# Performance work log

Hardware: AMD Instinct MI355X
Metric: run time of the kernel (lower is better)

## Reference

```python
import jax, jax.numpy as jnp
import numpy as np

NUM_EMBEDDINGS = 8192
EMBEDDING_DIM = 256
BETA = 0.25


def setup_inputs() -> dict:
    key = jax.random.key(0)
    k1, k2 = jax.random.split(key)
    z = jax.random.normal(k1, (16, 256, 32, 32), dtype=jnp.float32)
    # torch init: uniform(-1/K, 1/K)
    emb_w = jax.random.uniform(k2, (NUM_EMBEDDINGS, EMBEDDING_DIM),
                               dtype=jnp.float32,
                               minval=-1.0 / NUM_EMBEDDINGS,
                               maxval=1.0 / NUM_EMBEDDINGS)
    return {"z": z, "emb_w": emb_w}


def reference(z, emb_w):
    B, C, H, W = z.shape
    z_bhwc = jnp.transpose(z, (0, 2, 3, 1))          # [B,H,W,C]
    flat = z_bhwc.reshape(-1, C)                      # [N,C]
    d = (jnp.sum(flat * flat, axis=1, keepdims=True)
         + jnp.sum(emb_w * emb_w, axis=1)
         - 2.0 * flat @ emb_w.T)                      # [N,K]
    idx = jnp.argmin(d, axis=1)                       # [N]
    # direct gather (mathematically identical to one-hot @ emb_w)
    quantized = emb_w[idx].reshape(z_bhwc.shape)      # [B,H,W,C]
    q_latent_loss = jnp.mean((jax.lax.stop_gradient(quantized) - z_bhwc) ** 2)
    e_latent_loss = jnp.mean((quantized - jax.lax.stop_gradient(z_bhwc)) ** 2)
    loss = q_latent_loss + BETA * e_latent_loss
    # straight-through estimator
    quantized_st = z_bhwc + jax.lax.stop_gradient(quantized - z_bhwc)
    out = jnp.transpose(quantized_st, (0, 3, 1, 2))   # [B,C,H,W]
    return out, loss, idx.reshape(B, -1)
```

## Files before the change

### kernel.cpp

```cpp
#include <hip/hip_runtime.h>
#include <cstdint>
#include <cstddef>

#define N_PIX   16384
#define K_EMB   8192
#define DDIM    256

#define WS_A8       0
#define WS_E8       4194304
#define WS_KEYS     6291456
#define WS_ZSQ      23068672
#define WS_ESQ      23134208
#define WS_LOSS     23166976
#define WS_CNT      23166984

typedef float f32x4 __attribute__((ext_vector_type(4)));

__device__ __forceinline__ unsigned int f32_sortable(float f) {
    unsigned int u = __float_as_uint(f);
    return (u & 0x80000000u) ? ~u : (u | 0x80000000u);
}

__device__ __forceinline__ unsigned char f2fp8(float x) {
    unsigned ub = __float_as_uint(x);
    unsigned sgn = (ub >> 24) & 0x80u;
    unsigned b = ub & 0x7FFFFFFFu;
    unsigned out;
    if (__uint_as_float(b) < 0.015625f) {
        out = (unsigned)(int)rintf(__uint_as_float(b) * 512.0f);
    } else {
        unsigned r = b + 0x7FFFFu + ((b >> 20) & 1u);
        int er = (int)(r >> 23) - 127;
        out = (unsigned)(((er + 7) << 3) | ((r >> 20) & 7u));
    }
    return (unsigned char)(out | sgn);
}

#if defined(__has_builtin)
#if __has_builtin(__builtin_amdgcn_cvt_pk_fp8_f32)
#define HAVE_CVT_FP8 1
#endif
#endif

__device__ __forceinline__ unsigned pack4_fp8(float a, float b, float c, float d) {
#ifdef HAVE_CVT_FP8
    int pk = 0;
    pk = __builtin_amdgcn_cvt_pk_fp8_f32(a, b, pk, false);
    pk = __builtin_amdgcn_cvt_pk_fp8_f32(c, d, pk, true);
    return (unsigned)pk;
#else
    return (unsigned)f2fp8(a) | ((unsigned)f2fp8(b) << 8)
         | ((unsigned)f2fp8(c) << 16) | ((unsigned)f2fp8(d) << 24);
#endif
}

__device__ __forceinline__ void async16(const unsigned char* g, unsigned char* l) {
    __builtin_amdgcn_global_load_lds(
        (const __attribute__((address_space(1))) void*)g,
        (__attribute__((address_space(3))) void*)l, 16, 0, 0);
}

__device__ __forceinline__ float np_pairwise_sq256(const float* row) {
    float r[16];
#pragma unroll
    for (int j = 0; j < 16; ++j) r[j] = 0.f;
#pragma unroll
    for (int c = 0; c < 256; ++c) {
        float x  = row[c];
        float sq = __fmul_rn(x, x);
        int slot = ((c >> 7) << 3) | (c & 7);
        r[slot] = __fadd_rn(r[slot], sq);
    }
    float h0 = __fadd_rn(
        __fadd_rn(__fadd_rn(r[0], r[1]), __fadd_rn(r[2], r[3])),
        __fadd_rn(__fadd_rn(r[4], r[5]), __fadd_rn(r[6], r[7])));
    float h1 = __fadd_rn(
        __fadd_rn(__fadd_rn(r[8], r[9]), __fadd_rn(r[10], r[11])),
        __fadd_rn(__fadd_rn(r[12], r[13]), __fadd_rn(r[14], r[15])));
    return __fadd_rn(h0, h1);
}

__device__ __forceinline__ size_t cm_addr(int r, int c) {
    int ks = c >> 5;
    int h  = (c >> 4) & 1;
    int s  = h ^ ((r >> 2) & 1);
    return (size_t)ks * 4096 + (size_t)r * 32 + s * 16 + (c & 15);
}

__global__ __launch_bounds__(256) void prep_kernel(
        const float* __restrict__ z, const float* __restrict__ emb,
        unsigned char* __restrict__ Af8, unsigned char* __restrict__ Ef8,
        float* __restrict__ zsq, float* __restrict__ esq,
        double* __restrict__ lossAcc, unsigned* __restrict__ doneCnt) {
    __shared__ float tile[32][257];
    int blk = blockIdx.x;
    int t   = threadIdx.x;
    if (blk < 512) {
        int b   = blk >> 5;
        int hw0 = (blk & 31) * 32;
        const float* zb = z + (size_t)b * 262144 + hw0;
        int c0  = t >> 3;
        int px4 = t & 7;
#pragma unroll
        for (int cc = 0; cc < 8; ++cc) {
            int c = cc * 32 + c0;
            float4 v = *(const float4*)&zb[(size_t)c * 1024 + px4 * 4];
            tile[px4 * 4 + 0][c] = v.x;
            tile[px4 * 4 + 1][c] = v.y;
            tile[px4 * 4 + 2][c] = v.z;
            tile[px4 * 4 + 3][c] = v.w;
        }
        __syncthreads();
        int p0 = b * 1024 + hw0;
        int wv = t >> 6, lane = t & 63;
#pragma unroll
        for (int iter = 0; iter < 8; ++iter) {
            int pl = iter * 4 + wv;
            unsigned pk = pack4_fp8(tile[pl][lane * 4 + 0], tile[pl][lane * 4 + 1],
                                    tile[pl][lane * 4 + 2], tile[pl][lane * 4 + 3]);
            int p  = p0 + pl;
            int mb = p >> 7, r = p & 127;
            *(unsigned*)(Af8 + (size_t)mb * 32768 + cm_addr(r, lane * 4)) = pk;
        }
        if (t < 32) zsq[p0 + t] = np_pairwise_sq256(tile[t]);
        if (blk == 0 && t == 0) { *lossAcc = 0.0; *doneCnt = 0u; }
    } else {
        int k0 = (blk - 512) * 32;
        const float4* eg = (const float4*)(emb + (size_t)k0 * DDIM);
#pragma unroll
        for (int i = 0; i < 8; ++i) {
            int idx = i * 256 + t;
            int row = idx >> 6, c4 = idx & 63;
            float4 v = eg[idx];
            *(float4*)&tile[row][c4 * 4] = v;
        }
        __syncthreads();
#pragma unroll
        for (int i = 0; i < 8; ++i) {
            int idx = i * 256 + t;
            int row = idx >> 6, c4 = idx & 63;
            const float* rp = &tile[row][c4 * 4];
            int kg = k0 + row;
            int nb = kg >> 7, rr = kg & 127;
            *(unsigned*)(Ef8 + (size_t)nb * 32768 + cm_addr(rr, c4 * 4)) =
                pack4_fp8(rp[0] * 8192.0f, rp[1] * 8192.0f,
                          rp[2] * 8192.0f, rp[3] * 8192.0f);
        }
        if (t < 32) esq[k0 + t] = np_pairwise_sq256(tile[t]);
    }
}

__device__ __forceinline__ unsigned pack_key(float w) {
    float uf = __builtin_fmaf(w, -512.0f, 262144.0f);
    uf = fminf(uf, 524287.0f);
    unsigned u = (unsigned)uf;
    return (u << 13) | (__float_as_uint(w) & 0x1FFFu);
}

__global__ __launch_bounds__(256) void mfma_score_kernel(
        const unsigned char* __restrict__ Af8,
        const unsigned char* __restrict__ Ef8,
        unsigned int* __restrict__ keys) {
    union SM {
        struct { unsigned char As[8][4096]; unsigned char Bs[8][4096]; } k;
        struct { uint2 ep[128][33]; } e;
    };
    __shared__ SM sm;

    const int g  = blockIdx.x;
    const int mb = blockIdx.y;
    const int t = threadIdx.x;
    const int w = t >> 6, lane = t & 63;
    const int wm = w >> 1, wn = w & 1;
    const int quad = lane >> 4, l16 = lane & 15;

    const unsigned char* Ag = Af8 + (size_t)mb * 32768 + t * 16;
#pragma unroll
    for (int ks = 0; ks < 8; ++ks)
        async16(Ag + ks * 4096, &sm.k.As[ks][t * 16]);
    {
        const unsigned char* Eg = Ef8 + (size_t)(g * 4) * 32768 + t * 16;
#pragma unroll
        for (int ks = 0; ks < 8; ++ks)
            async16(Eg + ks * 4096, &sm.k.Bs[ks][t * 16]);
    }

    int aaddr[4], baddr[4];
#pragma unroll
    for (int fi = 0; fi < 4; ++fi) {
        int row = wm * 64 + fi * 16 + l16;
        int gg  = (quad >> 1) ^ ((row >> 2) & 1);
        aaddr[fi] = row * 32 + gg * 16 + (quad & 1) * 8;
    }
#pragma unroll
    for (int fj = 0; fj < 4; ++fj) {
        int row = wn * 64 + fj * 16 + l16;
        int gg  = (quad >> 1) ^ ((row >> 2) & 1);
        baddr[fj] = row * 32 + gg * 16 + (quad & 1) * 8;
    }

    __syncthreads();

    long long afr[4][8];
#pragma unroll
    for (int fi = 0; fi < 4; ++fi)
#pragma unroll
        for (int ks = 0; ks < 8; ++ks)
            afr[fi][ks] = *(const long long*)&sm.k.As[ks][aaddr[fi]];

    const float NEGINF = __int_as_float(0xFF800000);
    float t2a[16], t2b[16];
#pragma unroll
    for (int i = 0; i < 16; ++i) { t2a[i] = NEGINF; t2b[i] = NEGINF; }

#pragma unroll 1
    for (int j = 0; j < 4; ++j) {
        f32x4 acc[4][4];
#pragma unroll
        for (int i = 0; i < 4; ++i)
#pragma unroll
            for (int jj = 0; jj < 4; ++jj)
#pragma unroll
                for (int r = 0; r < 4; ++r) acc[i][jj][r] = 0.f;

#pragma unroll
        for (int ks = 0; ks < 8; ++ks) {
            long long bfr[4];
#pragma unroll
            for (int fj = 0; fj < 4; ++fj)
                bfr[fj] = *(const long long*)&sm.k.Bs[ks][baddr[fj]];
            __builtin_amdgcn_s_setprio(1);
#pragma unroll
            for (int fi = 0; fi < 4; ++fi)
#pragma unroll
                for (int fj = 0; fj < 4; ++fj)
                    acc[fi][fj] = __builtin_amdgcn_mfma_f32_16x16x32_fp8_fp8(
                        afr[fi][ks], bfr[fj], acc[fi][fj], 0, 0, 0);
            __builtin_amdgcn_s_setprio(0);
        }
        __syncthreads();

        if (j < 3) {
            const unsigned char* Eg =
                Ef8 + (size_t)(g * 4 + j + 1) * 32768 + t * 16;
#pragma unroll
            for (int ks = 0; ks < 8; ++ks)
                async16(Eg + ks * 4096, &sm.k.Bs[ks][t * 16]);
        }

        const int nb = g * 4 + j;
        const unsigned idx0 = (unsigned)(nb * 128 + wn * 64 + l16);
#pragma unroll
        for (int fi = 0; fi < 4; ++fi) {
#pragma unroll
            for (int r = 0; r < 4; ++r) {
                const int ai = fi * 4 + r;
                float a0 = t2a[ai], b0 = t2b[ai];
#pragma unroll
                for (int fj = 0; fj < 4; ++fj) {
                    float v = acc[fi][fj][r];
                    float wv = __uint_as_float(
                        (__float_as_uint(v) & 0xFFFFE000u) | (idx0 + fj * 16));
                    float mn = fminf(a0, wv);
                    a0 = fmaxf(a0, wv);
                    b0 = fmaxf(b0, mn);
                }
                t2a[ai] = a0; t2b[ai] = b0;
            }
        }
        __syncthreads();
    }

#pragma unroll
    for (int fi = 0; fi < 4; ++fi) {
#pragma unroll
        for (int r = 0; r < 4; ++r) {
            const int ai = fi * 4 + r;
            int row = wm * 64 + fi * 16 + quad * 4 + r;
            sm.e.ep[row][wn * 16 + l16] =
                make_uint2(pack_key(t2a[ai]), pack_key(t2b[ai]));
        }
    }
    __syncthreads();

    {
        int row = t >> 1, half = t & 1, h0 = half * 16;
        uint2 mv = sm.e.ep[row][h0];
#pragma unroll
        for (int i = 1; i < 16; ++i) {
            uint2 av = sm.e.ep[row][h0 + i];
            unsigned n0 = min(mv.x, av.x);
            unsigned n1 = min(max(mv.x, av.x), min(mv.y, av.y));
            mv.x = n0; mv.y = n1;
        }
        ((uint2*)keys)[(size_t)(g * 2 + half) * N_PIX + (mb * 128 + row)] = mv;
    }
}

__global__ __launch_bounds__(256) void final_kernel(
        const unsigned int* __restrict__ keys,
        const float* __restrict__ z, const float* __restrict__ emb,
        const float* __restrict__ zsq, const float* __restrict__ esq,
        float* __restrict__ out, float* __restrict__ idx_out,
        float* __restrict__ loss_out,
        double* __restrict__ lossAcc, unsigned* __restrict__ doneCnt) {
    __shared__ float ztile[16][260];
    __shared__ uint2 kt[16][33];
    __shared__ int   scand[16][64];
    __shared__ unsigned long long ckey[1024];
    __shared__ int   soff[17];
    __shared__ int   scnt[16];
    __shared__ int   pxmap[1024];
    __shared__ float szs[16];
    __shared__ int   sidx[16];

    int blk = blockIdx.x;
    int b = blk >> 6, hh = blk & 63;
    int t = threadIdx.x;
    int p0 = b * 1024 + hh * 16;
    const float* zb = z + (size_t)b * 262144 + hh * 16;
    {
        int px = t & 15, cb = t >> 4;
#pragma unroll
        for (int cc = 0; cc < 16; ++cc) {
            int c = cc * 16 + cb;
            ztile[px][c] = zb[(size_t)c * 1024 + px];
        }
    }
    {
        const uint2* kg = (const uint2*)keys;
#pragma unroll
        for (int itr = 0; itr < 2; ++itr) {
            int idx = itr * 256 + t;
            int px = idx & 15, hf = idx >> 4;
            kt[px][hf] = kg[(size_t)hf * N_PIX + p0 + px];
        }
    }
    if (t < 16) szs[t] = zsq[p0 + t];
    __syncthreads();

    {
        int wq = t >> 6, lane = t & 63;
#pragma unroll 1
        for (int i = 0; i < 4; ++i) {
            int px = wq * 4 + i;
            uint2 ka = (lane < 32) ? kt[px][lane] : make_uint2(~0u, ~0u);
            unsigned m = min(ka.x, ka.y);
#pragma unroll
            for (int off = 32; off >= 1; off >>= 1)
                m = min(m, (unsigned)__shfl_xor((int)m, off, 64));
            unsigned thr = (m >> 13) + 1600;

            bool h0 = (lane < 32) && ((ka.x >> 13) <= thr);
            bool h1 = (lane < 32) && ((ka.y >> 13) <= thr);
            unsigned long long m0 = __ballot(h0);
            unsigned long long m1 = __ballot(h1);
            int c0 = __popcll(m0);
            unsigned long long below = (lane == 63) ? ~0ull >> 1
                                     : ((1ull << lane) - 1);
            if (h0) scand[px][__popcll(m0 & below)] = (int)(ka.x & 0x1FFFu);
            if (h1) scand[px][c0 + __popcll(m1 & below)] = (int)(ka.y & 0x1FFFu);
            if (lane == 0) scnt[px] = c0 + __popcll(m1);
        }
    }
    __syncthreads();

    if (t < 64) {
        int v = (t < 16) ? scnt[t] : 0;
#pragma unroll
        for (int o = 1; o < 16; o <<= 1) {
            int u = __shfl_up(v, o, 64);
            if (t >= o) v += u;
        }
        if (t < 16) soff[t + 1] = v;
        if (t == 0) soff[0] = 0;
    }
    __syncthreads();
    int total = soff[16];
    for (int f = t; f < total; f += 256) {
        int lo = 0, hi = 15;
        while (lo < hi) {
            int mid = (lo + hi + 1) >> 1;
            if (soff[mid] <= f) lo = mid; else hi = mid - 1;
        }
        pxmap[f] = lo;
    }
    __syncthreads();

    {
        int gid = t >> 4, l16 = t & 15;
        const float4* emb4 = (const float4*)emb;
#pragma unroll 1
        for (int f = gid; f < total; f += 16) {
            int px = pxmap[f];
            int k  = scand[px][f - soff[px]];
            double d = 0.0;
#pragma unroll
            for (int q = 0; q < 4; ++q) {
                float4 ev = emb4[(size_t)k * 64 + q * 16 + l16];
                const float* zp = &ztile[px][(q * 16 + l16) * 4];
                d += (double)zp[0] * ev.x + (double)zp[1] * ev.y
                   + (double)zp[2] * ev.z + (double)zp[3] * ev.w;
            }
#pragma unroll
            for (int o = 1; o < 16; o <<= 1) d += __shfl_xor(d, o, 64);
            if (l16 == 0) {
                float df = (float)d;
                float s  = __fsub_rn(__fadd_rn(szs[px], esq[k]),
                                     __fmul_rn(2.0f, df));
                ckey[f] = ((unsigned long long)f32_sortable(s) << 32)
                        | (unsigned)k;
            }
        }
    }
    __syncthreads();

    {
        int cpx = t >> 4, ci = t & 15;
        unsigned long long best = ~0ull;
        for (int f = soff[cpx] + ci; f < soff[cpx + 1]; f += 16) {
            unsigned long long v = ckey[f];
            best = v < best ? v : best;
        }
#pragma unroll
        for (int o = 1; o < 16; o <<= 1) {
            unsigned long long ov =
                (unsigned long long)__shfl_xor((long long)best, o, 64);
            best = ov < best ? ov : best;
        }
        if (ci == 0) {
            int k = (int)(unsigned)(best & 0xffffffffu);
            sidx[cpx] = k;
            idx_out[p0 + cpx] = (float)k;
        }
    }
    __syncthreads();

    int px2 = t & 15, cy = t >> 4;
    int kk = sidx[px2];
    const float* er = emb + (size_t)kk * DDIM;
    float* ob = out + (size_t)b * 262144 + hh * 16;
    float local = 0.f;
#pragma unroll 4
    for (int it = 0; it < 16; ++it) {
        int c = it * 16 + cy;
        float q = er[c];
        float d = q - ztile[px2][c];
        ob[(size_t)c * 1024 + px2] = q;
        local += d * d;
    }
#pragma unroll
    for (int off = 32; off >= 1; off >>= 1) local += __shfl_down(local, off, 64);
    __shared__ float wsum[4];
    if ((t & 63) == 0) wsum[t >> 6] = local;
    __syncthreads();
    if (t == 0) {
        double s = (double)wsum[0] + (double)wsum[1]
                 + (double)wsum[2] + (double)wsum[3];
        atomicAdd(lossAcc, s);
        __threadfence();
        unsigned old = atomicAdd(doneCnt, 1u);
        if (old == 1023u) {
            double tot = atomicAdd(lossAcc, 0.0);
            *loss_out = (float)(tot * (1.25 / 4194304.0));
        }
    }
}

extern "C" void kernel_launch(void* const* d_in, const int* in_sizes, int n_in,
                              void* d_out, int out_size, void* d_ws, size_t ws_size,
                              hipStream_t stream) {
    const float* z   = (const float*)d_in[0];
    const float* emb = (const float*)d_in[1];
    float* out = (float*)d_out;
    char* ws = (char*)d_ws;

    unsigned char* Af8 = (unsigned char*)(ws + WS_A8);
    unsigned char* Ef8 = (unsigned char*)(ws + WS_E8);
    unsigned int* keys = (unsigned int*)(ws + WS_KEYS);
    float* zsq      = (float*)(ws + WS_ZSQ);
    float* esq      = (float*)(ws + WS_ESQ);
    double* lossAcc = (double*)(ws + WS_LOSS);
    unsigned* doneCnt = (unsigned*)(ws + WS_CNT);

    prep_kernel<<<768, 256, 0, stream>>>(z, emb, Af8, Ef8, zsq, esq,
                                         lossAcc, doneCnt);
    mfma_score_kernel<<<dim3(16, 128), 256, 0, stream>>>(Af8, Ef8, keys);
    final_kernel<<<1024, 256, 0, stream>>>(keys, z, emb, zsq, esq,
                                           out, out + 4194305, out + 4194304,
                                           lossAcc, doneCnt);
}
```

Measured before the change: 189.1 us.

## Load codebook fragments directly from global memory, drop shared B staging

The embedding (B) tile is no longer staged through shared memory with async copies and barriers. Each lane now reads its fp8 B fragments straight from global memory, with a one-step register prefetch across the k-steps. A fragments are reloaded from LDS each k-step instead of being held in 32 registers. This removes the per-iteration barriers and halves LDS use, which could allow more occupancy. The cost is many small uncoalesced 8-byte global loads whose latency may be poorly hidden.

```diff
diff --git a/kernel.cpp b/kernel.cpp
--- a/kernel.cpp
+++ b/kernel.cpp
@@ -162,7 +162,7 @@
         const unsigned char* __restrict__ Ef8,
         unsigned int* __restrict__ keys) {
     union SM {
-        struct { unsigned char As[8][4096]; unsigned char Bs[8][4096]; } k;
+        unsigned char As[8][4096];
         struct { uint2 ep[128][33]; } e;
     };
     __shared__ SM sm;
@@ -177,13 +177,7 @@
     const unsigned char* Ag = Af8 + (size_t)mb * 32768 + t * 16;
 #pragma unroll
     for (int ks = 0; ks < 8; ++ks)
-        async16(Ag + ks * 4096, &sm.k.As[ks][t * 16]);
-    {
-        const unsigned char* Eg = Ef8 + (size_t)(g * 4) * 32768 + t * 16;
-#pragma unroll
-        for (int ks = 0; ks < 8; ++ks)
-            async16(Eg + ks * 4096, &sm.k.Bs[ks][t * 16]);
-    }
+        async16(Ag + ks * 4096, &sm.As[ks][t * 16]);
 
     int aaddr[4], baddr[4];
 #pragma unroll
@@ -201,13 +195,6 @@
 
     __syncthreads();
 
-    long long afr[4][8];
-#pragma unroll
-    for (int fi = 0; fi < 4; ++fi)
-#pragma unroll
-        for (int ks = 0; ks < 8; ++ks)
-            afr[fi][ks] = *(const long long*)&sm.k.As[ks][aaddr[fi]];
-
     const float NEGINF = __int_as_float(0xFF800000);
     float t2a[16], t2b[16];
 #pragma unroll
@@ -215,6 +202,8 @@
 
 #pragma unroll 1
     for (int j = 0; j < 4; ++j) {
+        const unsigned char* Egj = Ef8 + (size_t)(g * 4 + j) * 32768;
+
         f32x4 acc[4][4];
 #pragma unroll
         for (int i = 0; i < 4; ++i)
@@ -223,29 +212,33 @@
 #pragma unroll
                 for (int r = 0; r < 4; ++r) acc[i][jj][r] = 0.f;
 
+        long long bcur[4], bnxt[4];
+#pragma unroll
+        for (int fj = 0; fj < 4; ++fj)
+            bcur[fj] = *(const long long*)(Egj + baddr[fj]);
+
 #pragma unroll
         for (int ks = 0; ks < 8; ++ks) {
-            long long bfr[4];
-#pragma unroll
-            for (int fj = 0; fj < 4; ++fj)
-                bfr[fj] = *(const long long*)&sm.k.Bs[ks][baddr[fj]];
+            if (ks < 7) {
+#pragma unroll
+                for (int fj = 0; fj < 4; ++fj)
+                    bnxt[fj] = *(const long long*)(Egj + (ks + 1) * 4096
+                                                   + baddr[fj]);
+            }
+            long long af[4];
+#pragma unroll
+            for (int fi = 0; fi < 4; ++fi)
+                af[fi] = *(const long long*)&sm.As[ks][aaddr[fi]];
             __builtin_amdgcn_s_setprio(1);
 #pragma unroll
             for (int fi = 0; fi < 4; ++fi)
 #pragma unroll
                 for (int fj = 0; fj < 4; ++fj)
                     acc[fi][fj] = __builtin_amdgcn_mfma_f32_16x16x32_fp8_fp8(
-                        afr[fi][ks], bfr[fj], acc[fi][fj], 0, 0, 0);
+                        af[fi], bcur[fj], acc[fi][fj], 0, 0, 0);
             __builtin_amdgcn_s_setprio(0);
-        }
-        __syncthreads();
-
-        if (j < 3) {
-            const unsigned char* Eg =
-                Ef8 + (size_t)(g * 4 + j + 1) * 32768 + t * 16;
-#pragma unroll
-            for (int ks = 0; ks < 8; ++ks)
-                async16(Eg + ks * 4096, &sm.k.Bs[ks][t * 16]);
+#pragma unroll
+            for (int fj = 0; fj < 4; ++fj) bcur[fj] = bnxt[fj];
         }
 
         const int nb = g * 4 + j;
@@ -268,8 +261,9 @@
                 t2a[ai] = a0; t2b[ai] = b0;
             }
         }
-        __syncthreads();
-    }
+    }
+
+    __syncthreads();
 
 #pragma unroll
     for (int fi = 0; fi < 4; ++fi) {
```

Result: slower. 217.3 us (+14.9%).
